# Kernel tuning notes

Measured on AMD Instinct MI355X. Metric: run time of the kernel, lower is better.

The kernel has to match this reference:

```python
import jax, jax.numpy as jnp
import numpy as np

B, T, E, H = 4, 1024, 768, 12
DH = E // H
MAXP = 64  # rel_max_positions per relation type
SCALE = DH ** -0.5


def _sinusoid_embed(max_pos, dim):
    # fairseq-style sinusoid table with padding row 0 zeroed
    num = max_pos + 1
    half = dim // 2
    freq = np.exp(np.arange(half) * -(np.log(10000.0) / (half - 1)))
    ang = np.arange(num)[:, None] * freq[None, :]
    emb = np.concatenate([np.sin(ang), np.cos(ang)], axis=1)
    emb[0] = 0.0
    return jnp.asarray(emb, dtype=jnp.float32)


def _xavier(key, out_d, in_d, gain):
    bound = gain * np.sqrt(6.0 / (in_d + out_d))
    return jax.random.uniform(key, (out_d, in_d), jnp.float32, -bound, bound)


def setup_inputs() -> dict:
    key = jax.random.key(0)
    ks = jax.random.split(key, 16)
    g = 1.0 / np.sqrt(2.0)
    inp = {
        'x': jax.random.normal(ks[0], (B, T, E), jnp.float32),
        'rel_pos0': jax.random.randint(ks[1], (T, T), 0, MAXP + 1),
        'rel_pos1': jax.random.randint(ks[2], (T, T), 0, MAXP + 1),
        'rel_emb0': _sinusoid_embed(MAXP, E),
        'rel_emb1': _sinusoid_embed(MAXP, E),
    }
    names = ['Wq_r', 'Wk_r', 'Wv_r', 'Wq_s', 'Wk_s', 'Wv_s', 'Wk2', 'Wv2', 'Wrel0', 'Wrel1']
    for i, n in enumerate(names):
        inp[n] = _xavier(ks[3 + i], E, E, g)
        inp[n.replace('W', 'b', 1)] = jnp.zeros((E,), jnp.float32)
    inp['Wo'] = _xavier(ks[13], E, E, 1.0)
    inp['bo'] = jnp.zeros((E,), jnp.float32)
    return inp


def _lin(x, W, b):
    return x @ W.T + b


def _heads(x):
    return x.reshape(x.shape[0], x.shape[1], H, DH).transpose(0, 2, 1, 3)  # [B,H,T,DH]


def reference(x, rel_pos0, rel_pos1, rel_emb0, rel_emb1,
              Wq_r, bq_r, Wk_r, bk_r, Wv_r, bv_r,
              Wq_s, bq_s, Wk_s, bk_s, Wv_s, bv_s,
              Wk2, bk2, Wv2, bv2,
              Wrel0, brel0, Wrel1, brel1, Wo, bo):
    # --- sum branch: plain attention producing per-position summaries ---
    qs = _heads(_lin(x, Wq_s, bq_s)) * SCALE
    ks_ = _heads(_lin(x, Wk_s, bk_s))
    vs = _heads(_lin(x, Wv_s, bv_s))
    attn_s = jax.nn.softmax(jnp.einsum('bhqd,bhkd->bhqk', qs, ks_), axis=-1)
    sum_x = jnp.einsum('bhqk,bhkd->bhqd', attn_s, vs).transpose(0, 2, 1, 3).reshape(B, T, E)
    # summaries re-projected as extra keys/values for the reg branch
    k2 = _heads(_lin(sum_x, Wk2, bk2))
    v2 = _heads(_lin(sum_x, Wv2, bv2))
    # --- reg branch with per-relation-type RPE score biases ---
    q = _heads(_lin(x, Wq_r, bq_r)) * SCALE
    k = _heads(_lin(x, Wk_r, bk_r))
    v = _heads(_lin(x, Wv_r, bv_r))
    s_reg = jnp.einsum('bhqd,bhkd->bhqk', q, k)
    for rel_pos, rel_emb, Wr, br in ((rel_pos0, rel_emb0, Wrel0, brel0),
                                     (rel_pos1, rel_emb1, Wrel1, brel1)):
        table = _lin(rel_emb, Wr, br).reshape(-1, H, DH)       # [P,H,DH]
        ts = jnp.einsum('bhqd,phd->bhqp', q, table)            # [B,H,T,P]
        idx = jnp.broadcast_to(rel_pos[None, None], (B, H, T, T))
        s_reg = s_reg + jnp.take_along_axis(ts, idx, axis=3)   # RPE gather
    s_sum = jnp.einsum('bhqd,bhkd->bhqk', q, k2)
    attn = jax.nn.softmax(jnp.concatenate([s_reg, s_sum], axis=-1), axis=-1)  # [B,H,T,2T]
    kv = jnp.concatenate([v, v2], axis=2)                       # [B,H,2T,DH]
    out = jnp.einsum('bhqk,bhkd->bhqd', attn, kv).transpose(0, 2, 1, 3).reshape(B, T, E)
    return _lin(out, Wo, bo)
```

## Files before the change

### kernel.cpp

```cpp
#include <hip/hip_runtime.h>
#include <hip/hip_bf16.h>
#include <stdint.h>


#define DEV __device__ __forceinline__

using f32x4 = __attribute__((ext_vector_type(4))) float;
using s16x8 = __attribute__((ext_vector_type(8))) short;
using s16x4 = __attribute__((ext_vector_type(4))) short;
using i32x4 = __attribute__((ext_vector_type(4))) int;
using u32x2 = __attribute__((ext_vector_type(2))) unsigned int;
using fvec4 = __attribute__((ext_vector_type(4))) float;
using u16 = unsigned short;

static constexpr int KD = 768;
static constexpr int PE = 4096 * 768;
static constexpr float QSCL = 0.18033688011112042f;

DEV u16 f2bf(float f) {
  uint32_t u = __builtin_bit_cast(uint32_t, f);
  u += 0x7FFF + ((u >> 16) & 1);
  return (u16)(u >> 16);
}
DEV float bf2f(u16 h) { return __builtin_bit_cast(float, (uint32_t)h << 16); }
DEV unsigned int cvtpk(float a, float b) {
  unsigned int r;
  asm("v_cvt_pk_bf16_f32 %0, %1, %2" : "=v"(r) : "v"(a), "v"(b));
  return r;
}

DEV void gload16(const void* g, void* l) {
  __builtin_amdgcn_global_load_lds((const __attribute__((address_space(1))) void*)g,
                                   (__attribute__((address_space(3))) void*)l, 16, 0, 0);
}
DEV f32x4 mfma16(s16x8 a, s16x8 b, f32x4 c) {
  return __builtin_amdgcn_mfma_f32_16x16x32_bf16(a, b, c, 0, 0, 0);
}

struct CastJobs {
  const float* src[14];
  u16* dst[14];
  int n[14];
};
__global__ __launch_bounds__(256) void cast_bf16_kernel(CastJobs J) {
  const int job = blockIdx.y;
  const int i = (blockIdx.x * 256 + threadIdx.x) * 8;
  if (i >= J.n[job]) return;
  const fvec4* s = (const fvec4*)(J.src[job] + i);
  fvec4 a = s[0], b = s[1];
  s16x8 o;
  o[0] = (short)f2bf(a[0]); o[1] = (short)f2bf(a[1]);
  o[2] = (short)f2bf(a[2]); o[3] = (short)f2bf(a[3]);
  o[4] = (short)f2bf(b[0]); o[5] = (short)f2bf(b[1]);
  o[6] = (short)f2bf(b[2]); o[7] = (short)f2bf(b[3]);
  *(s16x8*)(J.dst[job] + i) = o;
}

__global__ __launch_bounds__(256) void pack_rp_kernel(const int* rp0, const int* rp1, u16* outp) {
  const int i = (blockIdx.x * 256 + threadIdx.x) * 8;
  i32x4 a0 = *(const i32x4*)(rp0 + i), a1 = *(const i32x4*)(rp0 + i + 4);
  i32x4 b0 = *(const i32x4*)(rp1 + i), b1 = *(const i32x4*)(rp1 + i + 4);
  s16x8 o;
  o[0] = (short)(a0[0] | (b0[0] << 8));
  o[1] = (short)(a0[1] | (b0[1] << 8));
  o[2] = (short)(a0[2] | (b0[2] << 8));
  o[3] = (short)(a0[3] | (b0[3] << 8));
  o[4] = (short)(a1[0] | (b1[0] << 8));
  o[5] = (short)(a1[1] | (b1[1] << 8));
  o[6] = (short)(a1[2] | (b1[2] << 8));
  o[7] = (short)(a1[3] | (b1[3] << 8));
  *(s16x8*)(outp + i) = o;
}

struct GemmP {
  const u16* A;
  const u16* Bw;
  const float* bias[6];
  u16* out_bf;
  float* out_f;
  const u16* A2;
  const u16* Bw2;
  u16* out2;
  int epi;
};

__global__ __launch_bounds__(256) void gemm_bt(GemmP p) {
  __shared__ __align__(16) u16 As[128 * 64];
  __shared__ __align__(16) u16 Bs[128 * 64];
  const int tid = threadIdx.x;
  const int m0 = blockIdx.x * 128, n0 = blockIdx.y * 128;
  const int zz = blockIdx.z;
  const u16* Ag = (zz ? p.A2 : p.A) + (size_t)m0 * KD;
  const u16* Bg = (zz ? p.Bw2 : p.Bw) + (size_t)n0 * KD;
  const int lane = tid & 63, wid = tid >> 6;
  const int wm = (wid >> 1) * 64, wn = (wid & 1) * 64;
  const int lhi = lane >> 4, llo = lane & 15;

  uint ldso[4], srco[4];
#pragma unroll
  for (int j = 0; j < 4; ++j) {
    uint o = tid * 16 + j * 4096;
    uint row = o >> 7, kc = (o >> 4) & 7;
    ldso[j] = o;
    srco[j] = row * KD + ((kc ^ (row & 7)) << 3);
  }

  f32x4 acc[4][4] = {};

  for (int kt = 0; kt < 12; ++kt) {
    const int k0 = kt * 64;
#pragma unroll
    for (int j = 0; j < 4; ++j) gload16(Ag + srco[j] + k0, (char*)As + ldso[j]);
#pragma unroll
    for (int j = 0; j < 4; ++j) gload16(Bg + srco[j] + k0, (char*)Bs + ldso[j]);
    __syncthreads();
#pragma unroll
    for (int kf = 0; kf < 2; ++kf) {
      s16x8 av[4], bv[4];
#pragma unroll
      for (int mf = 0; mf < 4; ++mf) {
        int r = wm + mf * 16 + llo;
        av[mf] = *(const s16x8*)&As[r * 64 + ((((kf << 2) | lhi) ^ (r & 7)) << 3)];
      }
#pragma unroll
      for (int nf = 0; nf < 4; ++nf) {
        int r = wn + nf * 16 + llo;
        bv[nf] = *(const s16x8*)&Bs[r * 64 + ((((kf << 2) | lhi) ^ (r & 7)) << 3)];
      }
#pragma unroll
      for (int mf = 0; mf < 4; ++mf)
#pragma unroll
        for (int nf = 0; nf < 4; ++nf)
          acc[mf][nf] = mfma16(av[mf], bv[nf], acc[mf][nf]);
    }
    __syncthreads();
  }

  const int epi = p.epi;
#pragma unroll
  for (int nf = 0; nf < 4; ++nf) {
    const int n = n0 + wn + nf * 16 + llo;
    int proj = 0, n1 = n, hh, dd;
    float bias, scale = 1.0f;
    if (epi <= 1) {
      proj = n / 768; n1 = n - proj * 768;
      hh = n1 >> 6; dd = n1 & 63;
      bias = p.bias[proj][n1];
      if (epi == 0 && (proj == 0 || proj == 3)) scale = QSCL;
    } else {
      hh = n >> 6; dd = n & 63;
      bias = p.bias[zz ? 1 : 0][n];
    }
#pragma unroll
    for (int mf = 0; mf < 4; ++mf) {
      f32x4 c = acc[mf][nf];
      const int mb = m0 + wm + mf * 16 + lhi * 4;
      if (epi == 3) {
#pragma unroll
        for (int r = 0; r < 4; ++r)
          p.out_f[(size_t)(mb + r) * 768 + n] = c[r] + bias;
      } else if (epi == 2) {
        u16* ob = zz ? p.out2 : p.out_bf;
#pragma unroll
        for (int r = 0; r < 4; ++r) {
          int m = mb + r;
          if (m < 80) ob[((size_t)hh * 80 + m) * 64 + dd] = f2bf(c[r] + bias);
        }
      } else {
        const bool vlay = (epi == 0) ? (proj == 2 || proj == 5) : (proj == 1);
        if (vlay) {
          const int b = mb >> 10, t = mb & 1023;
          const int bh = b * 12 + hh;
          s16x4 o4;
          o4[0] = (short)f2bf((c[0] + bias) * scale);
          o4[1] = (short)f2bf((c[1] + bias) * scale);
          o4[2] = (short)f2bf((c[2] + bias) * scale);
          o4[3] = (short)f2bf((c[3] + bias) * scale);
          *(s16x4*)&p.out_bf[(size_t)proj * PE + ((size_t)(bh * 64 + dd)) * 1024 + t] = o4;
        } else {
#pragma unroll
          for (int r = 0; r < 4; ++r) {
            int m = mb + r;
            int b = m >> 10, t = m & 1023;
            int bh = b * 12 + hh;
            p.out_bf[(size_t)proj * PE + ((size_t)(bh * 1024 + t)) * 64 + dd] =
                f2bf((c[r] + bias) * scale);
          }
        }
      }
    }
  }
}

__global__ __launch_bounds__(256) void sum_attn_kernel(const u16* Qs, const u16* Ks,
                                                       const u16* Vst, u16* sum_x) {
  __shared__ __align__(16) u16 kbuf[64 * 64];
  __shared__ __align__(16) u16 vbuf[64 * 64];
  __shared__ __align__(16) u16 pbuf[4][16 * 72];
  const int tid = threadIdx.x, lane = tid & 63, w = tid >> 6;
  const int lhi = lane >> 4, llo = lane & 15;
  const int bid = blockIdx.x;
  const int vid = (bid & 7) * 96 + (bid >> 3);
  const int qt = vid & 15, bh = vid >> 4;
  const int qbase = qt * 64 + w * 16;

  const u16* Qg = Qs + ((size_t)bh * 1024 + qbase + llo) * 64;
  s16x8 aq0 = *(const s16x8*)(Qg + lhi * 8);
  s16x8 aq1 = *(const s16x8*)(Qg + 32 + lhi * 8);

  f32x4 accO[4] = {};
  float mrun = -1e30f, lrun = 0.f;

  uint so[2], srow[2], sswz[2];
#pragma unroll
  for (int j = 0; j < 2; ++j) {
    uint o = tid * 16 + j * 4096;
    so[j] = o; srow[j] = o >> 7;
    sswz[j] = (((o >> 4) & 7) ^ (srow[j] & 7)) << 3;
  }
  const u16* Kg = Ks + (size_t)bh * 65536;
  const u16* Vg = Vst + (size_t)bh * 65536;

  for (int kt = 0; kt < 16; ++kt) {
#pragma unroll
    for (int j = 0; j < 2; ++j) {
      gload16(Kg + (size_t)kt * 4096 + srow[j] * 64 + sswz[j], (char*)kbuf + so[j]);
      gload16(Vg + (size_t)srow[j] * 1024 + kt * 64 + sswz[j], (char*)vbuf + so[j]);
    }
    __syncthreads();

    f32x4 s[4];
    __builtin_amdgcn_s_setprio(1);
#pragma unroll
    for (int kc4 = 0; kc4 < 4; ++kc4) {
      f32x4 c = {};
#pragma unroll
      for (int kf = 0; kf < 2; ++kf) {
        int kr = kc4 * 16 + llo;
        s16x8 bk = *(const s16x8*)&kbuf[kr * 64 + ((((kf << 2) | lhi) ^ (kr & 7)) << 3)];
        c = mfma16(bk, kf ? aq1 : aq0, c);
      }
      s[kc4] = c;
    }
    __builtin_amdgcn_s_setprio(0);

    float smx = s[0][0];
#pragma unroll
    for (int kc4 = 0; kc4 < 4; ++kc4)
#pragma unroll
      for (int r = 0; r < 4; ++r) smx = fmaxf(smx, s[kc4][r]);
    if (!__all(smx <= mrun + 8.0f)) {
      float mall = fmaxf(smx, __shfl_xor(smx, 16, 64));
      mall = fmaxf(mall, __shfl_xor(mall, 32, 64));
      float mn = fmaxf(mrun, mall);
      float corr = exp2f(mrun - mn);
      mrun = mn;
      lrun *= corr;
      float cf[4];
#pragma unroll
      for (int r = 0; r < 4; ++r) cf[r] = __shfl(corr, lhi * 4 + r, 64);
#pragma unroll
      for (int dc = 0; dc < 4; ++dc)
#pragma unroll
        for (int r = 0; r < 4; ++r) accO[dc][r] *= cf[r];
    }
    float ls = 0.f;
#pragma unroll
    for (int kc4 = 0; kc4 < 4; ++kc4) {
      float p0 = exp2f(s[kc4][0] - mrun), p1 = exp2f(s[kc4][1] - mrun);
      float p2 = exp2f(s[kc4][2] - mrun), p3 = exp2f(s[kc4][3] - mrun);
      ls += (p0 + p1) + (p2 + p3);
      u32x2 pk; pk[0] = cvtpk(p0, p1); pk[1] = cvtpk(p2, p3);
      *(u32x2*)&pbuf[w][llo * 72 + kc4 * 16 + lhi * 4] = pk;
    }
    lrun += ls;

    __builtin_amdgcn_s_setprio(1);
#pragma unroll
    for (int kf = 0; kf < 2; ++kf) {
      s16x8 ap = *(const s16x8*)&pbuf[w][llo * 72 + kf * 32 + lhi * 8];
#pragma unroll
      for (int dc = 0; dc < 4; ++dc) {
        int dr = dc * 16 + llo;
        s16x8 bv = *(const s16x8*)&vbuf[dr * 64 + ((((kf << 2) | lhi) ^ (dr & 7)) << 3)];
        accO[dc] = mfma16(ap, bv, accO[dc]);
      }
    }
    __builtin_amdgcn_s_setprio(0);
    __syncthreads();
  }

  lrun += __shfl_xor(lrun, 16, 64);
  lrun += __shfl_xor(lrun, 32, 64);
  float linv[4];
#pragma unroll
  for (int r = 0; r < 4; ++r) linv[r] = 1.0f / __shfl(lrun, lhi * 4 + r, 64);

  const int b = bh / 12, hh = bh - b * 12;
#pragma unroll
  for (int dc = 0; dc < 4; ++dc)
#pragma unroll
    for (int r = 0; r < 4; ++r) {
      int q = qbase + lhi * 4 + r;
      sum_x[((size_t)b * 1024 + q) * 768 + hh * 64 + dc * 16 + llo] = f2bf(accO[dc][r] * linv[r]);
    }
}

__global__ __launch_bounds__(256) void reg_attn_kernel(
    const u16* Qr, const u16* Kr, const u16* Vrt,
    const u16* K2, const u16* V2t,
    const u16* tab0, const u16* tab1,
    const u16* rpk, u16* attn_out) {
  __shared__ __align__(16) u16 kbuf[64 * 64];
  __shared__ __align__(16) u16 vbuf[64 * 64];
  __shared__ __align__(16) u16 tsb0[64 * 80];
  __shared__ __align__(16) u16 tsb1[64 * 80];
  __shared__ __align__(16) u16 pbuf[4][16 * 72];
  const int tid = threadIdx.x, lane = tid & 63, w = tid >> 6;
  const int lhi = lane >> 4, llo = lane & 15;
  const int bid = blockIdx.x;
  const int vid = (bid & 7) * 96 + (bid >> 3);
  const int qt = vid & 15, bh = vid >> 4;
  const int b = bh / 12, hh = bh - b * 12;
  const int qbase = qt * 64 + w * 16;
  const int qloc = w * 16 + llo;

  const u16* Qg = Qr + ((size_t)bh * 1024 + qbase + llo) * 64;
  s16x8 aq0 = *(const s16x8*)(Qg + lhi * 8);
  s16x8 aq1 = *(const s16x8*)(Qg + 32 + lhi * 8);

#pragma unroll
  for (int tt = 0; tt < 2; ++tt) {
    const u16* tb = tt ? tab1 : tab0;
    u16* dst = tt ? tsb1 : tsb0;
#pragma unroll
    for (int pf = 0; pf < 5; ++pf) {
      f32x4 c = {};
#pragma unroll
      for (int kf = 0; kf < 2; ++kf) {
        s16x8 bt = *(const s16x8*)(tb + ((size_t)hh * 80 + pf * 16 + llo) * 64 + kf * 32 + lhi * 8);
        c = mfma16(bt, kf ? aq1 : aq0, c);
      }
      u32x2 pk; pk[0] = cvtpk(c[0], c[1]); pk[1] = cvtpk(c[2], c[3]);
      *(u32x2*)&dst[(w * 16 + llo) * 80 + pf * 16 + lhi * 4] = pk;
    }
  }
  __syncthreads();

  f32x4 accO[4] = {};
  float mrun = -1e30f, lrun = 0.f;

  uint so[2], srow[2], sswz[2];
#pragma unroll
  for (int j = 0; j < 2; ++j) {
    uint o = tid * 16 + j * 4096;
    so[j] = o; srow[j] = o >> 7;
    sswz[j] = (((o >> 4) & 7) ^ (srow[j] & 7)) << 3;
  }
  const u16* KgA = Kr + (size_t)bh * 65536;
  const u16* KgB = K2 + (size_t)bh * 65536;
  const u16* VgA = Vrt + (size_t)bh * 65536;
  const u16* VgB = V2t + (size_t)bh * 65536;

  auto tile = [&](const u16* Kg, const u16* Vg, int kk, bool gather) {
#pragma unroll
    for (int j = 0; j < 2; ++j) {
      gload16(Kg + (size_t)kk * 4096 + srow[j] * 64 + sswz[j], (char*)kbuf + so[j]);
      gload16(Vg + (size_t)srow[j] * 1024 + kk * 64 + sswz[j], (char*)vbuf + so[j]);
    }
    s16x4 pp4[4];
    if (gather) {
#pragma unroll
      for (int kc4 = 0; kc4 < 4; ++kc4)
        pp4[kc4] = *(const s16x4*)&rpk[(size_t)(qbase + llo) * 1024 + kk * 64 + kc4 * 16 + lhi * 4];
    }
    __syncthreads();

    f32x4 s[4];
    __builtin_amdgcn_s_setprio(1);
#pragma unroll
    for (int kc4 = 0; kc4 < 4; ++kc4) {
      f32x4 c = {};
#pragma unroll
      for (int kf = 0; kf < 2; ++kf) {
        int kr = kc4 * 16 + llo;
        s16x8 bk = *(const s16x8*)&kbuf[kr * 64 + ((((kf << 2) | lhi) ^ (kr & 7)) << 3)];
        c = mfma16(bk, kf ? aq1 : aq0, c);
      }
      s[kc4] = c;
    }
    __builtin_amdgcn_s_setprio(0);

    if (gather) {
#pragma unroll
      for (int kc4 = 0; kc4 < 4; ++kc4)
#pragma unroll
        for (int r = 0; r < 4; ++r) {
          int v = (u16)pp4[kc4][r];
          s[kc4][r] += bf2f(tsb0[qloc * 80 + (v & 255)]) + bf2f(tsb1[qloc * 80 + (v >> 8)]);
        }
    }

    float smx = s[0][0];
#pragma unroll
    for (int kc4 = 0; kc4 < 4; ++kc4)
#pragma unroll
      for (int r = 0; r < 4; ++r) smx = fmaxf(smx, s[kc4][r]);
    if (!__all(smx <= mrun + 8.0f)) {
      float mall = fmaxf(smx, __shfl_xor(smx, 16, 64));
      mall = fmaxf(mall, __shfl_xor(mall, 32, 64));
      float mn = fmaxf(mrun, mall);
      float corr = exp2f(mrun - mn);
      mrun = mn;
      lrun *= corr;
      float cf[4];
#pragma unroll
      for (int r = 0; r < 4; ++r) cf[r] = __shfl(corr, lhi * 4 + r, 64);
#pragma unroll
      for (int dc = 0; dc < 4; ++dc)
#pragma unroll
        for (int r = 0; r < 4; ++r) accO[dc][r] *= cf[r];
    }
    float ls = 0.f;
#pragma unroll
    for (int kc4 = 0; kc4 < 4; ++kc4) {
      float p0 = exp2f(s[kc4][0] - mrun), p1 = exp2f(s[kc4][1] - mrun);
      float p2 = exp2f(s[kc4][2] - mrun), p3 = exp2f(s[kc4][3] - mrun);
      ls += (p0 + p1) + (p2 + p3);
      u32x2 pk; pk[0] = cvtpk(p0, p1); pk[1] = cvtpk(p2, p3);
      *(u32x2*)&pbuf[w][llo * 72 + kc4 * 16 + lhi * 4] = pk;
    }
    lrun += ls;

    __builtin_amdgcn_s_setprio(1);
#pragma unroll
    for (int kf = 0; kf < 2; ++kf) {
      s16x8 ap = *(const s16x8*)&pbuf[w][llo * 72 + kf * 32 + lhi * 8];
#pragma unroll
      for (int dc = 0; dc < 4; ++dc) {
        int dr = dc * 16 + llo;
        s16x8 bv = *(const s16x8*)&vbuf[dr * 64 + ((((kf << 2) | lhi) ^ (dr & 7)) << 3)];
        accO[dc] = mfma16(ap, bv, accO[dc]);
      }
    }
    __builtin_amdgcn_s_setprio(0);
    __syncthreads();
  };

  for (int kt = 0; kt < 16; ++kt) tile(KgA, VgA, kt, true);
  for (int kt = 0; kt < 16; ++kt) tile(KgB, VgB, kt, false);

  lrun += __shfl_xor(lrun, 16, 64);
  lrun += __shfl_xor(lrun, 32, 64);
  float linv[4];
#pragma unroll
  for (int r = 0; r < 4; ++r) linv[r] = 1.0f / __shfl(lrun, lhi * 4 + r, 64);

#pragma unroll
  for (int dc = 0; dc < 4; ++dc)
#pragma unroll
    for (int r = 0; r < 4; ++r) {
      int q = qbase + lhi * 4 + r;
      attn_out[((size_t)b * 1024 + q) * 768 + hh * 64 + dc * 16 + llo] = f2bf(accO[dc][r] * linv[r]);
    }
}

extern "C" void kernel_launch(void* const* d_in, const int* in_sizes, int n_in,
                              void* d_out, int out_size, void* d_ws, size_t ws_size,
                              hipStream_t stream) {
  (void)in_sizes; (void)n_in; (void)out_size; (void)ws_size;
  const float* x     = (const float*)d_in[0];
  const int*   rp0   = (const int*)d_in[1];
  const int*   rp1   = (const int*)d_in[2];
  const float* re0   = (const float*)d_in[3];
  const float* re1   = (const float*)d_in[4];
  const float* Wq_r  = (const float*)d_in[5];  const float* bq_r = (const float*)d_in[6];
  const float* Wk_r  = (const float*)d_in[7];  const float* bk_r = (const float*)d_in[8];
  const float* Wv_r  = (const float*)d_in[9];  const float* bv_r = (const float*)d_in[10];
  const float* Wq_s  = (const float*)d_in[11]; const float* bq_s = (const float*)d_in[12];
  const float* Wk_s  = (const float*)d_in[13]; const float* bk_s = (const float*)d_in[14];
  const float* Wv_s  = (const float*)d_in[15]; const float* bv_s = (const float*)d_in[16];
  const float* Wk2   = (const float*)d_in[17]; const float* bk2  = (const float*)d_in[18];
  const float* Wv2   = (const float*)d_in[19]; const float* bv2  = (const float*)d_in[20];
  const float* Wrel0 = (const float*)d_in[21]; const float* brel0 = (const float*)d_in[22];
  const float* Wrel1 = (const float*)d_in[23]; const float* brel1 = (const float*)d_in[24];
  const float* Wo    = (const float*)d_in[25]; const float* bo   = (const float*)d_in[26];
  float* out = (float*)d_out;

  char* wp = (char*)d_ws;
  auto carve = [&](size_t bytes) {
    char* r = wp;
    wp += (bytes + 255) & ~(size_t)255;
    return r;
  };
  u16* xb     = (u16*)carve((size_t)PE * 2);
  u16* Wcat1  = (u16*)carve((size_t)4608 * 768 * 2);
  u16* Wcat2  = (u16*)carve((size_t)1536 * 768 * 2);
  u16* Wrel0b = (u16*)carve((size_t)768 * 768 * 2);
  u16* Wrel1b = (u16*)carve((size_t)768 * 768 * 2);
  u16* Wob    = (u16*)carve((size_t)768 * 768 * 2);
  u16* relA0  = (u16*)carve((size_t)128 * 768 * 2);
  u16* relA1  = (u16*)carve((size_t)128 * 768 * 2);
  u16* qkv    = (u16*)carve((size_t)6 * PE * 2);
  u16* k2v2   = (u16*)carve((size_t)2 * PE * 2);
  u16* tb0    = (u16*)carve((size_t)12 * 80 * 64 * 2);
  u16* tb1    = (u16*)carve((size_t)12 * 80 * 64 * 2);
  u16* rpk    = (u16*)carve((size_t)1024 * 1024 * 2);
  u16* sumx   = (u16*)carve((size_t)PE * 2);
  u16* aout   = (u16*)carve((size_t)PE * 2);

  const int wn_ = 768 * 768;
  CastJobs J;
  const float* srcs[14] = {x, Wq_r, Wk_r, Wv_r, Wq_s, Wk_s, Wv_s, Wk2, Wv2, Wrel0, Wrel1, Wo, re0, re1};
  u16* dsts[14] = {xb, Wcat1, Wcat1 + wn_, Wcat1 + 2 * wn_, Wcat1 + 3 * wn_, Wcat1 + 4 * wn_,
                   Wcat1 + 5 * wn_, Wcat2, Wcat2 + wn_, Wrel0b, Wrel1b, Wob, relA0, relA1};
  int ns[14] = {PE, wn_, wn_, wn_, wn_, wn_, wn_, wn_, wn_, wn_, wn_, wn_, 65 * 768, 65 * 768};
  for (int i = 0; i < 14; ++i) { J.src[i] = srcs[i]; J.dst[i] = dsts[i]; J.n[i] = ns[i]; }
  cast_bf16_kernel<<<dim3(1536, 14), 256, 0, stream>>>(J);

  pack_rp_kernel<<<dim3(512), 256, 0, stream>>>(rp0, rp1, rpk);

  GemmP g1{};
  g1.A = xb; g1.Bw = Wcat1;
  g1.bias[0] = bq_r; g1.bias[1] = bk_r; g1.bias[2] = bv_r;
  g1.bias[3] = bq_s; g1.bias[4] = bk_s; g1.bias[5] = bv_s;
  g1.out_bf = qkv; g1.epi = 0;
  gemm_bt<<<dim3(32, 36), 256, 0, stream>>>(g1);

  GemmP gt{};
  gt.A = relA0; gt.Bw = Wrel0b; gt.bias[0] = brel0; gt.out_bf = tb0;
  gt.A2 = relA1; gt.Bw2 = Wrel1b; gt.bias[1] = brel1; gt.out2 = tb1;
  gt.epi = 2;
  gemm_bt<<<dim3(1, 6, 2), 256, 0, stream>>>(gt);

  sum_attn_kernel<<<dim3(768), 256, 0, stream>>>(qkv + (size_t)3 * PE, qkv + (size_t)4 * PE,
                                                 qkv + (size_t)5 * PE, sumx);

  GemmP g2{};
  g2.A = sumx; g2.Bw = Wcat2; g2.bias[0] = bk2; g2.bias[1] = bv2;
  g2.out_bf = k2v2; g2.epi = 1;
  gemm_bt<<<dim3(32, 12), 256, 0, stream>>>(g2);

  reg_attn_kernel<<<dim3(768), 256, 0, stream>>>(qkv, qkv + (size_t)PE, qkv + (size_t)2 * PE,
                                                 k2v2, k2v2 + (size_t)PE, tb0, tb1, rpk, aout);

  GemmP gf{};
  gf.A = aout; gf.Bw = Wob; gf.bias[0] = bo; gf.out_f = out; gf.epi = 3;
  gemm_bt<<<dim3(32, 6), 256, 0, stream>>>(gf);
}
```

Baseline: 366.3 us.

## Stage GEMM epilogue through LDS for vector stores; XOR-swizzle P buffer

Non-V-layout projection blocks now write their biased, scaled bf16 results into shared memory with a swizzled layout, then issue 16-byte coalesced stores into the head-major output instead of scattered 2-byte stores. The attention kernels replace the padded 72-stride P buffer with an XOR-swizzled 64-stride layout and add an explicit LDS wait plus a scheduling barrier before the PV MFMAs. The aim is less uncoalesced global write traffic and fewer LDS bank conflicts, at the cost of an extra barrier and LDS round trip in the GEMM epilogue. The code assumes each 128-column block lies inside a single projection, which holds because 768 is a multiple of 128.

```diff
diff --git a/kernel.cpp b/kernel.cpp
--- a/kernel.cpp
+++ b/kernel.cpp
@@ -85,8 +85,9 @@
 };
 
 __global__ __launch_bounds__(256) void gemm_bt(GemmP p) {
-  __shared__ __align__(16) u16 As[128 * 64];
-  __shared__ __align__(16) u16 Bs[128 * 64];
+  __shared__ __align__(16) u16 smem[128 * 128];
+  u16* As = smem;
+  u16* Bs = smem + 8192;
   const int tid = threadIdx.x;
   const int m0 = blockIdx.x * 128, n0 = blockIdx.y * 128;
   const int zz = blockIdx.z;
@@ -110,9 +111,9 @@
   for (int kt = 0; kt < 12; ++kt) {
     const int k0 = kt * 64;
 #pragma unroll
-    for (int j = 0; j < 4; ++j) gload16(Ag + srco[j] + k0, (char*)As + ldso[j]);
-#pragma unroll
-    for (int j = 0; j < 4; ++j) gload16(Bg + srco[j] + k0, (char*)Bs + ldso[j]);
+    for (int j = 0; j < 4; ++j) gload16(Ag + srco[j] + k0, (char*)smem + ldso[j]);
+#pragma unroll
+    for (int j = 0; j < 4; ++j) gload16(Bg + srco[j] + k0, (char*)smem + 16384 + ldso[j]);
     __syncthreads();
 #pragma unroll
     for (int kf = 0; kf < 2; ++kf) {
@@ -137,16 +138,55 @@
   }
 
   const int epi = p.epi;
+  const int proj0 = (epi <= 1) ? (n0 / 768) : 0;
+  const bool vlay_blk = (epi == 0 && (proj0 == 2 || proj0 == 5)) || (epi == 1 && proj0 == 1);
+
+  if (epi <= 1 && !vlay_blk) {
+    const float scale = (epi == 0 && (proj0 == 0 || proj0 == 3)) ? QSCL : 1.0f;
+#pragma unroll
+    for (int nf = 0; nf < 4; ++nf) {
+      const int nl = wn + nf * 16 + llo;
+      const float bias = p.bias[proj0][n0 + nl - proj0 * 768];
+      const int nb = nl >> 3, ns = nl & 7;
+#pragma unroll
+      for (int mf = 0; mf < 4; ++mf) {
+        const f32x4 c = acc[mf][nf];
+        const int mb_ = wm + mf * 16 + lhi * 4;
+#pragma unroll
+        for (int r = 0; r < 4; ++r) {
+          const int ml = mb_ + r;
+          smem[ml * 128 + ((nb ^ (ml & 7)) << 3) + ns] = f2bf((c[r] + bias) * scale);
+        }
+      }
+    }
+    __syncthreads();
+    const int j = tid & 7;
+    const int base = tid >> 3;
+    const int seg = base & 1;
+    const int m_base = base >> 1;
+    const int hh = (n0 + seg * 64 - proj0 * 768) >> 6;
+#pragma unroll
+    for (int w8 = 0; w8 < 8; ++w8) {
+      const int ml = m_base + w8 * 16;
+      const int bblk = seg * 8 + j;
+      s16x8 v = *(const s16x8*)&smem[ml * 128 + ((bblk ^ (ml & 7)) << 3)];
+      const int mg = m0 + ml;
+      const int bi = mg >> 10, t = mg & 1023;
+      const int bh = bi * 12 + hh;
+      *(s16x8*)&p.out_bf[(size_t)proj0 * PE + ((size_t)(bh * 1024 + t)) * 64 + j * 8] = v;
+    }
+    return;
+  }
+
 #pragma unroll
   for (int nf = 0; nf < 4; ++nf) {
     const int n = n0 + wn + nf * 16 + llo;
     int proj = 0, n1 = n, hh, dd;
     float bias, scale = 1.0f;
     if (epi <= 1) {
-      proj = n / 768; n1 = n - proj * 768;
+      proj = proj0; n1 = n - proj * 768;
       hh = n1 >> 6; dd = n1 & 63;
       bias = p.bias[proj][n1];
-      if (epi == 0 && (proj == 0 || proj == 3)) scale = QSCL;
     } else {
       hh = n >> 6; dd = n & 63;
       bias = p.bias[zz ? 1 : 0][n];
@@ -167,26 +207,14 @@
           if (m < 80) ob[((size_t)hh * 80 + m) * 64 + dd] = f2bf(c[r] + bias);
         }
       } else {
-        const bool vlay = (epi == 0) ? (proj == 2 || proj == 5) : (proj == 1);
-        if (vlay) {
-          const int b = mb >> 10, t = mb & 1023;
-          const int bh = b * 12 + hh;
-          s16x4 o4;
-          o4[0] = (short)f2bf((c[0] + bias) * scale);
-          o4[1] = (short)f2bf((c[1] + bias) * scale);
-          o4[2] = (short)f2bf((c[2] + bias) * scale);
-          o4[3] = (short)f2bf((c[3] + bias) * scale);
-          *(s16x4*)&p.out_bf[(size_t)proj * PE + ((size_t)(bh * 64 + dd)) * 1024 + t] = o4;
-        } else {
-#pragma unroll
-          for (int r = 0; r < 4; ++r) {
-            int m = mb + r;
-            int b = m >> 10, t = m & 1023;
-            int bh = b * 12 + hh;
-            p.out_bf[(size_t)proj * PE + ((size_t)(bh * 1024 + t)) * 64 + dd] =
-                f2bf((c[r] + bias) * scale);
-          }
-        }
+        const int b = mb >> 10, t = mb & 1023;
+        const int bh = b * 12 + hh;
+        s16x4 o4;
+        o4[0] = (short)f2bf((c[0] + bias) * scale);
+        o4[1] = (short)f2bf((c[1] + bias) * scale);
+        o4[2] = (short)f2bf((c[2] + bias) * scale);
+        o4[3] = (short)f2bf((c[3] + bias) * scale);
+        *(s16x4*)&p.out_bf[(size_t)proj * PE + ((size_t)(bh * 64 + dd)) * 1024 + t] = o4;
       }
     }
   }
@@ -196,7 +224,7 @@
                                                        const u16* Vst, u16* sum_x) {
   __shared__ __align__(16) u16 kbuf[64 * 64];
   __shared__ __align__(16) u16 vbuf[64 * 64];
-  __shared__ __align__(16) u16 pbuf[4][16 * 72];
+  __shared__ __align__(16) u16 pbuf[4][16 * 64];
   const int tid = threadIdx.x, lane = tid & 63, w = tid >> 6;
   const int lhi = lane >> 4, llo = lane & 15;
   const int bid = blockIdx.x;
@@ -271,14 +299,19 @@
       float p2 = exp2f(s[kc4][2] - mrun), p3 = exp2f(s[kc4][3] - mrun);
       ls += (p0 + p1) + (p2 + p3);
       u32x2 pk; pk[0] = cvtpk(p0, p1); pk[1] = cvtpk(p2, p3);
-      *(u32x2*)&pbuf[w][llo * 72 + kc4 * 16 + lhi * 4] = pk;
+      const int kb = (kc4 << 1) | (lhi >> 1);
+      *(u32x2*)&pbuf[w][llo * 64 + ((kb ^ (llo & 7)) << 3) + ((lhi & 1) << 2)] = pk;
     }
     lrun += ls;
 
+    asm volatile("s_waitcnt lgkmcnt(0)" ::: "memory");
+    __builtin_amdgcn_sched_barrier(0);
+
     __builtin_amdgcn_s_setprio(1);
 #pragma unroll
     for (int kf = 0; kf < 2; ++kf) {
-      s16x8 ap = *(const s16x8*)&pbuf[w][llo * 72 + kf * 32 + lhi * 8];
+      const int kb = (kf << 2) | lhi;
+      s16x8 ap = *(const s16x8*)&pbuf[w][llo * 64 + ((kb ^ (llo & 7)) << 3)];
 #pragma unroll
       for (int dc = 0; dc < 4; ++dc) {
         int dr = dc * 16 + llo;
@@ -315,7 +348,7 @@
   __shared__ __align__(16) u16 vbuf[64 * 64];
   __shared__ __align__(16) u16 tsb0[64 * 80];
   __shared__ __align__(16) u16 tsb1[64 * 80];
-  __shared__ __align__(16) u16 pbuf[4][16 * 72];
+  __shared__ __align__(16) u16 pbuf[4][16 * 64];
   const int tid = threadIdx.x, lane = tid & 63, w = tid >> 6;
   const int lhi = lane >> 4, llo = lane & 15;
   const int bid = blockIdx.x;
@@ -428,14 +461,19 @@
       float p2 = exp2f(s[kc4][2] - mrun), p3 = exp2f(s[kc4][3] - mrun);
       ls += (p0 + p1) + (p2 + p3);
       u32x2 pk; pk[0] = cvtpk(p0, p1); pk[1] = cvtpk(p2, p3);
-      *(u32x2*)&pbuf[w][llo * 72 + kc4 * 16 + lhi * 4] = pk;
+      const int kb = (kc4 << 1) | (lhi >> 1);
+      *(u32x2*)&pbuf[w][llo * 64 + ((kb ^ (llo & 7)) << 3) + ((lhi & 1) << 2)] = pk;
     }
     lrun += ls;
 
+    asm volatile("s_waitcnt lgkmcnt(0)" ::: "memory");
+    __builtin_amdgcn_sched_barrier(0);
+
     __builtin_amdgcn_s_setprio(1);
 #pragma unroll
     for (int kf = 0; kf < 2; ++kf) {
-      s16x8 ap = *(const s16x8*)&pbuf[w][llo * 72 + kf * 32 + lhi * 8];
+      const int kb = (kf << 2) | lhi;
+      s16x8 ap = *(const s16x8*)&pbuf[w][llo * 64 + ((kb ^ (llo & 7)) << 3)];
 #pragma unroll
       for (int dc = 0; dc < 4; ++dc) {
         int dr = dc * 16 + llo;
```

New measurement: 359.3 us. About the same (-1.9%).
